# Performance work log

Hardware: AMD Instinct MI355X
Metric: run time of the kernel (lower is better)

Reference implementation:

```python
import jax, jax.numpy as jnp
import numpy as np

CHEB_K = 3


def cheb_gcn(x, node_emb, w_pool, b_pool):
    # x: [B, N, C], node_emb: [N, D], w_pool: [D, K, C, O], b_pool: [D, O]
    n = node_emb.shape[0]
    A = jax.nn.softmax(jax.nn.relu(node_emb @ node_emb.T), axis=1)  # [N, N]
    supports = [jnp.eye(n, dtype=x.dtype), A]
    for _ in range(2, CHEB_K):
        supports.append(2.0 * A @ supports[-1] - supports[-2])
    S = jnp.stack(supports, axis=0)  # [K, N, N]
    weights = jnp.einsum('nd,dkio->nkio', node_emb, w_pool)  # [N, K, C, O]
    bias = node_emb @ b_pool  # [N, O]
    x_g = jnp.einsum('knm,bmc->bnkc', S, x)  # [B, N, K, C]
    return jnp.einsum('bnki,nkio->bno', x_g, weights) + bias


def setup_inputs() -> dict:
    key = jax.random.key(0)
    ks = jax.random.split(key, 7)
    B, N, DIN, DOUT, E = 64, 1024, 64, 64, 16
    C = DIN + DOUT
    return {
        'x': jax.random.normal(ks[0], (B, N, DIN), jnp.float32),
        'state': jax.random.normal(ks[1], (B, N, DOUT), jnp.float32),
        'node_embeddings': jax.random.normal(ks[2], (N, E), jnp.float32),
        'W_gate': jax.random.normal(ks[3], (E, CHEB_K, C, 2 * DOUT), jnp.float32) * 0.1,
        'b_gate': jax.random.normal(ks[4], (E, 2 * DOUT), jnp.float32) * 0.1,
        'W_update': jax.random.normal(ks[5], (E, CHEB_K, C, DOUT), jnp.float32) * 0.1,
        'b_update': jax.random.normal(ks[6], (E, DOUT), jnp.float32) * 0.1,
    }


def reference(x, state, node_embeddings, W_gate, b_gate, W_update, b_update):
    hidden = state.shape[-1]
    inp = jnp.concatenate([x, state], axis=-1)  # [B, N, DIN+DOUT]
    z_r = jax.nn.sigmoid(cheb_gcn(inp, node_embeddings, W_gate, b_gate))
    z, r = z_r[..., :hidden], z_r[..., hidden:]
    cand = jnp.concatenate([x, r * state], axis=-1)
    h_hat = jnp.tanh(cheb_gcn(cand, node_embeddings, W_update, b_update))
    return z * state + (1.0 - z) * h_hat
```

## Files before the change

### kernel.cpp

```cpp
#include <hip/hip_runtime.h>
#include <hip/hip_bf16.h>
#include <math.h>

#define B_ 64
#define N_ 1024
#define E_ 16

typedef unsigned short ushort_t;
typedef __attribute__((ext_vector_type(8))) short bf16x8;
typedef __attribute__((ext_vector_type(4))) float f32x4;

__device__ __forceinline__ float sigmoidf_(float x) {
  return 1.0f / (1.0f + __expf(-x));
}
__device__ __forceinline__ ushort_t f2bf(float f) {
  unsigned int u = __float_as_uint(f);
  u = (u + 0x7fffu + ((u >> 16) & 1u)) >> 16;
  return (ushort_t)u;
}
__device__ __forceinline__ float bf2f(ushort_t h) { return __uint_as_float((unsigned)h << 16); }
__device__ __forceinline__ void gload16(const void* g, void* l) {
  __builtin_amdgcn_global_load_lds(
      (const __attribute__((address_space(1))) unsigned int*)g,
      (__attribute__((address_space(3))) unsigned int*)l, 16, 0, 0);
}

__global__ __launch_bounds__(256) void compute_A_kernel(const float* __restrict__ emb,
                                                        ushort_t* __restrict__ Ah,
                                                        ushort_t* __restrict__ Al) {
  __shared__ float embn[E_];
  __shared__ float red[256];
  const int n = blockIdx.x;
  const int t = threadIdx.x;
  if (t < E_) embn[t] = emb[n * E_ + t];
  __syncthreads();
  float s[4];
#pragma unroll
  for (int j = 0; j < 4; ++j) {
    const int m = j * 256 + t;
    const float* em = emb + m * E_;
    float acc = 0.f;
#pragma unroll
    for (int d = 0; d < E_; ++d) acc = fmaf(embn[d], em[d], acc);
    s[j] = fmaxf(acc, 0.f);
  }
  float mx = fmaxf(fmaxf(s[0], s[1]), fmaxf(s[2], s[3]));
  red[t] = mx;
  __syncthreads();
  for (int off = 128; off > 0; off >>= 1) {
    if (t < off) red[t] = fmaxf(red[t], red[t + off]);
    __syncthreads();
  }
  mx = red[0];
  __syncthreads();
  float e[4], lsum = 0.f;
#pragma unroll
  for (int j = 0; j < 4; ++j) { e[j] = __expf(s[j] - mx); lsum += e[j]; }
  red[t] = lsum;
  __syncthreads();
  for (int off = 128; off > 0; off >>= 1) {
    if (t < off) red[t] += red[t + off];
    __syncthreads();
  }
  const float inv = 1.0f / red[0];
#pragma unroll
  for (int j = 0; j < 4; ++j) {
    const float v = e[j] * inv;
    ushort_t h = f2bf(v);
    Ah[n * N_ + j * 256 + t] = h;
    Al[n * N_ + j * 256 + t] = f2bf(v - bf2f(h));
  }
}

__global__ __launch_bounds__(256) void transpose_A_kernel(const ushort_t* __restrict__ src1,
                                                          ushort_t* __restrict__ dst1,
                                                          const ushort_t* __restrict__ src2,
                                                          ushort_t* __restrict__ dst2) {
  __shared__ ushort_t tile[128][130];
  const int t = threadIdx.x;
  const int r0 = blockIdx.y << 7, c0 = blockIdx.x << 7;
  const ushort_t* src = src1;
  ushort_t* dst = dst1;
#pragma unroll
  for (int p = 0; p < 2; ++p) {
    if (p) { src = src2; dst = dst2; __syncthreads(); }
#pragma unroll
    for (int it = 0; it < 8; ++it) {
      const int id = it * 256 + t;
      const int row = id >> 4, ch = (id & 15) << 3;
      *(uint4*)&tile[row][ch] = *(const uint4*)&src[(size_t)(r0 + row) * 1024 + c0 + ch];
    }
    __syncthreads();
#pragma unroll
    for (int it = 0; it < 8; ++it) {
      const int id = it * 256 + t;
      const int row = id >> 4, ch = (id & 15) << 3;
      ushort_t v[8];
#pragma unroll
      for (int u = 0; u < 8; ++u) v[u] = tile[ch + u][row];
      *(uint4*)&dst[(size_t)(c0 + row) * 1024 + r0 + ch] = *(const uint4*)v;
    }
    __syncthreads();
  }
}

__global__ __launch_bounds__(256) void build_T0t_kernel(const float* __restrict__ xA,
                                                        const float* __restrict__ xB,
                                                        ushort_t* __restrict__ Th,
                                                        ushort_t* __restrict__ Tl) {
  __shared__ float tile[128][129];
  const int t = threadIdx.x;
  const int b = blockIdx.y;
  const int n0 = blockIdx.x << 7;
  const int c4 = (t & 31) << 2, nl = t >> 5;
#pragma unroll
  for (int p = 0; p < 16; ++p) {
    const int n = nl + (p << 3);
    const float4 v = (c4 < 64)
        ? *(const float4*)&xA[((size_t)b << 16) + ((size_t)(n0 + n) << 6) + c4]
        : *(const float4*)&xB[((size_t)b << 16) + ((size_t)(n0 + n) << 6) + c4 - 64];
    tile[c4 + 0][n] = v.x; tile[c4 + 1][n] = v.y;
    tile[c4 + 2][n] = v.z; tile[c4 + 3][n] = v.w;
  }
  __syncthreads();
  const int c = t >> 1, nc = (t & 1) << 6;
  const size_t obase = ((size_t)(b << 7) + c) * 1024 + n0 + nc;
#pragma unroll
  for (int u = 0; u < 64; u += 4) {
    ushort4 h, l;
    float v0 = tile[c][nc + u + 0], v1 = tile[c][nc + u + 1];
    float v2 = tile[c][nc + u + 2], v3 = tile[c][nc + u + 3];
    h.x = f2bf(v0); l.x = f2bf(v0 - bf2f(h.x));
    h.y = f2bf(v1); l.y = f2bf(v1 - bf2f(h.y));
    h.z = f2bf(v2); l.z = f2bf(v2 - bf2f(h.z));
    h.w = f2bf(v3); l.w = f2bf(v3 - bf2f(h.w));
    *(ushort4*)&Th[obase + u] = h;
    *(ushort4*)&Tl[obase + u] = l;
  }
}

__global__ __launch_bounds__(256) void build_T0s_kernel(const float* __restrict__ rs,
                                                        ushort_t* __restrict__ Th,
                                                        ushort_t* __restrict__ Tl) {
  __shared__ float tile[64][129];
  const int t = threadIdx.x;
  const int b = blockIdx.y;
  const int n0 = blockIdx.x << 7;
  const int c4 = (t & 15) << 2, nl = t >> 4;
#pragma unroll
  for (int p = 0; p < 8; ++p) {
    const int n = nl + (p << 4);
    const float4 v = *(const float4*)&rs[((size_t)b << 16) + ((size_t)(n0 + n) << 6) + c4];
    tile[c4 + 0][n] = v.x; tile[c4 + 1][n] = v.y;
    tile[c4 + 2][n] = v.z; tile[c4 + 3][n] = v.w;
  }
  __syncthreads();
  const int c = t >> 2, nc = (t & 3) << 5;
  const size_t obase = ((size_t)(b << 6) + c) * 1024 + n0 + nc;
#pragma unroll
  for (int u = 0; u < 32; u += 4) {
    ushort4 h, l;
    float v0 = tile[c][nc + u + 0], v1 = tile[c][nc + u + 1];
    float v2 = tile[c][nc + u + 2], v3 = tile[c][nc + u + 3];
    h.x = f2bf(v0); l.x = f2bf(v0 - bf2f(h.x));
    h.y = f2bf(v1); l.y = f2bf(v1 - bf2f(h.y));
    h.z = f2bf(v2); l.z = f2bf(v2 - bf2f(h.z));
    h.w = f2bf(v3); l.w = f2bf(v3 - bf2f(h.w));
    *(ushort4*)&Th[obase + u] = h;
    *(ushort4*)&Tl[obase + u] = l;
  }
}

template <int MODE, int SPAN>
__global__ __launch_bounds__(256, 2) void mfma_gemm_kernel(
    const ushort_t* __restrict__ Ah, const ushort_t* __restrict__ Al,
    const ushort_t* __restrict__ Bh, const ushort_t* __restrict__ Bl,
    ushort_t* __restrict__ OutH, ushort_t* __restrict__ OutL) {
  __shared__ ushort_t smem[4 * 128 * 64];
  ushort_t* Ah_s = smem;
  ushort_t* Al_s = smem + 8192;
  ushort_t* Bh_s = smem + 16384;
  ushort_t* Bl_s = smem + 24576;
  const int t = threadIdx.x;
  const int wave = t >> 6, lane = t & 63;
  const int n0 = blockIdx.y << 7;
  const int bcol = blockIdx.x;
  const int j0 = bcol << 7;
  const int wr = wave >> 1, wc = wave & 1;
  const int fr = lane & 15, fk = lane >> 4;

  f32x4 acc[4][4];
#pragma unroll
  for (int i = 0; i < 4; ++i)
#pragma unroll
    for (int j = 0; j < 4; ++j) acc[i][j] = (f32x4){0.f, 0.f, 0.f, 0.f};

  const int rsub = lane >> 3;
  const int cp = lane & 7;
  const int selem = (((cp << 4) ^ (rsub << 4)) >> 1);

  for (int k0 = 0; k0 < 1024; k0 += 64) {
    __syncthreads();
#pragma unroll
    for (int i = 0; i < 4; ++i) {
      const int q = (wave << 2) + i;
      const int row = (q << 3) + rsub;
      const int lo = (q << 9) + lane * 8;
      const size_t ga = (size_t)(n0 + row) * 1024 + k0 + selem;
      const size_t gb = (size_t)(j0 + row) * 1024 + k0 + selem;
      gload16(Ah + ga, Ah_s + lo);
      gload16(Al + ga, Al_s + lo);
      gload16(Bh + gb, Bh_s + lo);
      gload16(Bl + gb, Bl_s + lo);
    }
    __syncthreads();
#pragma unroll
    for (int ks = 0; ks < 2; ++ks) {
      bf16x8 ah[4], al[4], bh[4], bl[4];
#pragma unroll
      for (int mi = 0; mi < 4; ++mi) {
        const int r = (wr << 6) + (mi << 4) + fr;
        const int kb = ((ks << 6) + (fk << 4)) ^ ((r & 7) << 4);
        ah[mi] = *(const bf16x8*)((const char*)Ah_s + r * 128 + kb);
        al[mi] = *(const bf16x8*)((const char*)Al_s + r * 128 + kb);
      }
#pragma unroll
      for (int nj = 0; nj < 4; ++nj) {
        const int r = (wc << 6) + (nj << 4) + fr;
        const int kb = ((ks << 6) + (fk << 4)) ^ ((r & 7) << 4);
        bh[nj] = *(const bf16x8*)((const char*)Bh_s + r * 128 + kb);
        bl[nj] = *(const bf16x8*)((const char*)Bl_s + r * 128 + kb);
      }
#pragma unroll
      for (int mi = 0; mi < 4; ++mi)
#pragma unroll
        for (int nj = 0; nj < 4; ++nj) {
          acc[mi][nj] = __builtin_amdgcn_mfma_f32_16x16x32_bf16(ah[mi], bh[nj], acc[mi][nj], 0, 0, 0);
          acc[mi][nj] = __builtin_amdgcn_mfma_f32_16x16x32_bf16(ah[mi], bl[nj], acc[mi][nj], 0, 0, 0);
          acc[mi][nj] = __builtin_amdgcn_mfma_f32_16x16x32_bf16(al[mi], bh[nj], acc[mi][nj], 0, 0, 0);
        }
    }
  }

  __syncthreads();
  ushort_t* hiT = smem;
  ushort_t* loT = smem + 16384;
#pragma unroll
  for (int mi = 0; mi < 4; ++mi) {
    const int nl = (wr << 6) + (mi << 4) + (fk << 2);
#pragma unroll
    for (int nj = 0; nj < 4; ++nj) {
      const int jl = (wc << 6) + (nj << 4) + fr;
      const f32x4 vv = acc[mi][nj];
#pragma unroll
      for (int r = 0; r < 4; ++r) {
        const float v = (MODE == 1) ? 2.0f * vv[r] : vv[r];
        const ushort_t h = f2bf(v);
        hiT[(nl + r) * 128 + jl] = h;
        loT[(nl + r) * 128 + jl] = f2bf(v - bf2f(h));
      }
    }
  }
  __syncthreads();
  const int soff = (n0 >= 1024) ? 128 : 0;
  const int n0e = n0 & 1023;
#pragma unroll
  for (int rr = 0; rr < 8; ++rr) {
    const int id = rr * 256 + t;
    const int nl = id >> 4, ch = id & 15;
    size_t dstE;
    if (MODE == 1) {
      dstE = (size_t)(n0 + nl) * 1024 + j0 + ch * 8;
    } else if (SPAN == 128) {
      dstE = ((size_t)(n0e + nl) * 64 + bcol) * 256 + soff + ch * 8;
    } else {
      const int bb = bcol * 2 + (ch >> 3);
      dstE = ((size_t)(n0e + nl) * 64 + bb) * 256 + soff + 64 + (ch & 7) * 8;
    }
    *(uint4*)&OutH[dstE] = *(const uint4*)((const char*)hiT + nl * 256 + ch * 16);
    *(uint4*)&OutL[dstE] = *(const uint4*)((const char*)loT + nl * 256 + ch * 16);
  }
}

template <int OW>
__global__ __launch_bounds__(256) void wpt_kernel(const float* __restrict__ Wp,
                                                  float* __restrict__ WpT) {
  const int idx = blockIdx.x * 256 + threadIdx.x;
  const int ki = idx % 384;
  const int k = ki >> 7, i = ki & 127;
  const int o = idx / 384;
  float v[16];
#pragma unroll
  for (int d = 0; d < 16; ++d) v[d] = Wp[((size_t)d * 384 + ki) * OW + o];
  if (k == 0) {
#pragma unroll
    for (int d = 0; d < 16; ++d) v[d] -= Wp[((size_t)d * 384 + 256 + i) * OW + o];
  }
  float* dst = WpT + (size_t)idx * 16;
#pragma unroll
  for (int q = 0; q < 4; ++q) *(float4*)&dst[q * 4] = *(const float4*)&v[q * 4];
}

__global__ __launch_bounds__(384) void wcombine5_kernel(const float* __restrict__ emb,
                                                        const float* __restrict__ WpT,
                                                        ushort_t* __restrict__ WtH,
                                                        ushort_t* __restrict__ WtL) {
  __shared__ float embs[256 * 16];
  __shared__ ushort_t sH[8 * 384];
  __shared__ ushort_t sL[8 * 384];
  const int t = threadIdx.x;
  const int o = blockIdx.y;
  const int n0 = blockIdx.x << 8;
  for (int i = t; i < 1024; i += 384)
    *(float4*)&embs[i * 4] = *(const float4*)&emb[(size_t)n0 * 16 + i * 4];
  float wreg[16];
  {
    const float* src = WpT + (size_t)o * 6144 + t * 16;
#pragma unroll
    for (int q = 0; q < 4; ++q) *(float4*)&wreg[q * 4] = *(const float4*)&src[q * 4];
  }
  __syncthreads();
  for (int g = 0; g < 32; ++g) {
#pragma unroll
    for (int nl = 0; nl < 8; ++nl) {
      const float* e = &embs[(g * 8 + nl) * 16];
      float a = 0.f;
#pragma unroll
      for (int d = 0; d < 16; ++d) a = fmaf(e[d], wreg[d], a);
      const ushort_t h = f2bf(a);
      sH[nl * 384 + t] = h;
      sL[nl * 384 + t] = f2bf(a - bf2f(h));
    }
    __syncthreads();
    const size_t ob = ((size_t)o * 1024 + n0 + g * 8) * 384 + t * 8;
    *(uint4*)&WtH[ob] = *(const uint4*)&sH[t * 8];
    *(uint4*)&WtL[ob] = *(const uint4*)&sL[t * 8];
    __syncthreads();
  }
}

template <int MODE>
__global__ __launch_bounds__(256, 2) void pernode_mfma_kernel(
    const float* __restrict__ xA, const float* __restrict__ xB,
    const ushort_t* __restrict__ XpH, const ushort_t* __restrict__ XpL,
    const ushort_t* __restrict__ WtH, const ushort_t* __restrict__ WtL,
    const float* __restrict__ emb, const float* __restrict__ bsrc, int bstride,
    const float* __restrict__ state, const float* __restrict__ zb,
    float* __restrict__ dst) {
  __shared__ ushort_t xh_s[64 * 128];
  __shared__ ushort_t xl_s[64 * 128];
  __shared__ ushort_t wh_s[64 * 128];
  __shared__ ushort_t wl_s[64 * 128];
  __shared__ float embn[E_];
  __shared__ float bias[64];
  const int n = blockIdx.x;
  const int t = threadIdx.x;
  if (t < E_) embn[t] = emb[n * E_ + t];
  __syncthreads();
  if (t < 64) {
    float a = 0.f;
#pragma unroll
    for (int d = 0; d < E_; ++d) a = fmaf(embn[d], bsrc[d * bstride + t], a);
    bias[t] = a;
  }
  const int wave = t >> 6, lane = t & 63;
  const int fr = lane & 15, fq = lane >> 4;
  f32x4 acc[4];
#pragma unroll
  for (int i = 0; i < 4; ++i) acc[i] = (f32x4){0.f, 0.f, 0.f, 0.f};

#pragma unroll
  for (int s = 0; s < 3; ++s) {
    __syncthreads();
    if (s == 0) {
      const int b = t >> 2, q = t & 3;
      const float* srcp = (q < 2)
          ? xA + ((size_t)b << 16) + ((size_t)n << 6) + (q << 5)
          : xB + ((size_t)b << 16) + ((size_t)n << 6) + ((q - 2) << 5);
      float v[32];
#pragma unroll
      for (int j = 0; j < 8; ++j) *(float4*)&v[j * 4] = *(const float4*)&srcp[j * 4];
      const int swz = (b & 7) << 4;
#pragma unroll
      for (int jc = 0; jc < 4; ++jc) {
        unsigned int hh[4], ll[4];
#pragma unroll
        for (int e = 0; e < 4; ++e) {
          const float a0 = v[jc * 8 + 2 * e], a1 = v[jc * 8 + 2 * e + 1];
          const ushort_t h0 = f2bf(a0), h1 = f2bf(a1);
          const ushort_t l0 = f2bf(a0 - bf2f(h0)), l1 = f2bf(a1 - bf2f(h1));
          hh[e] = (unsigned)h0 | ((unsigned)h1 << 16);
          ll[e] = (unsigned)l0 | ((unsigned)l1 << 16);
        }
        const int dstb = b * 256 + (((q << 6) + (jc << 4)) ^ swz);
        *(uint4*)((char*)xh_s + dstb) = make_uint4(hh[0], hh[1], hh[2], hh[3]);
        *(uint4*)((char*)xl_s + dstb) = make_uint4(ll[0], ll[1], ll[2], ll[3]);
      }
    } else {
#pragma unroll
      for (int r = 0; r < 4; ++r) {
        const int id = r * 256 + t;
        const int row = id >> 4, ch = id & 15;
        const int selem = (((ch << 4) ^ ((row & 7) << 4)) >> 1);
        const size_t so = ((size_t)n * 64 + row) * 256 + (s - 1) * 128 + selem;
        gload16(XpH + so, xh_s + id * 8);
        gload16(XpL + so, xl_s + id * 8);
      }
    }
#pragma unroll
    for (int r = 0; r < 4; ++r) {
      const int id = r * 256 + t;
      const int row = id >> 4, ch = id & 15;
      const int selem = (((ch << 4) ^ ((row & 7) << 4)) >> 1);
      const size_t so = ((size_t)row * 1024 + n) * 384 + s * 128 + selem;
      gload16(WtH + so, wh_s + id * 8);
      gload16(WtL + so, wl_s + id * 8);
    }
    __syncthreads();
#pragma unroll
    for (int ks = 0; ks < 4; ++ks) {
      bf16x8 ah[4], al[4];
#pragma unroll
      for (int mi = 0; mi < 4; ++mi) {
        const int r = (mi << 4) + fr;
        const int kb = ((ks << 6) + (fq << 4)) ^ ((r & 7) << 4);
        ah[mi] = *(const bf16x8*)((const char*)xh_s + r * 256 + kb);
        al[mi] = *(const bf16x8*)((const char*)xl_s + r * 256 + kb);
      }
      const int rw = (wave << 4) + fr;
      const int kbw = ((ks << 6) + (fq << 4)) ^ ((rw & 7) << 4);
      const bf16x8 wh = *(const bf16x8*)((const char*)wh_s + rw * 256 + kbw);
      const bf16x8 wl = *(const bf16x8*)((const char*)wl_s + rw * 256 + kbw);
#pragma unroll
      for (int mi = 0; mi < 4; ++mi) {
        acc[mi] = __builtin_amdgcn_mfma_f32_16x16x32_bf16(ah[mi], wh, acc[mi], 0, 0, 0);
        acc[mi] = __builtin_amdgcn_mfma_f32_16x16x32_bf16(al[mi], wh, acc[mi], 0, 0, 0);
        acc[mi] = __builtin_amdgcn_mfma_f32_16x16x32_bf16(ah[mi], wl, acc[mi], 0, 0, 0);
      }
    }
  }

  const int o = (wave << 4) + fr;
  const float bia = bias[o];
#pragma unroll
  for (int mi = 0; mi < 4; ++mi) {
    const int b0 = (mi << 4) + (fq << 2);
    const f32x4 vv = acc[mi];
#pragma unroll
    for (int r = 0; r < 4; ++r) {
      const int b = b0 + r;
      const size_t base = ((size_t)b << 16) + ((size_t)n << 6);
      const float a = vv[r] + bia;
      if (MODE == 0) {
        dst[base + o] = sigmoidf_(a);
      } else if (MODE == 1) {
        dst[base + o] = sigmoidf_(a) * state[base + o];
      } else {
        const float z = zb[base + o], st = state[base + o];
        dst[base + o] = z * st + (1.f - z) * tanhf(a);
      }
    }
  }
}

extern "C" void kernel_launch(void* const* d_in, const int* in_sizes, int n_in,
                              void* d_out, int out_size, void* d_ws, size_t ws_size,
                              hipStream_t stream) {
  const float* x     = (const float*)d_in[0];
  const float* state = (const float*)d_in[1];
  const float* emb   = (const float*)d_in[2];
  const float* Wg    = (const float*)d_in[3];
  const float* bg    = (const float*)d_in[4];
  const float* Wu    = (const float*)d_in[5];
  const float* bu    = (const float*)d_in[6];
  float* out = (float*)d_out;

  char* w = (char*)d_ws;
  ushort_t* AhS  = (ushort_t*)(w);
  ushort_t* AlS  = (ushort_t*)(w + ((size_t)4 << 20));
  ushort_t* Ath  = (ushort_t*)(w + ((size_t)8 << 20));
  ushort_t* Atl  = (ushort_t*)(w + ((size_t)10 << 20));
  ushort_t* T0th = (ushort_t*)(w + ((size_t)12 << 20));
  ushort_t* T0tl = (ushort_t*)(w + ((size_t)28 << 20));
  ushort_t* XpH  = (ushort_t*)(w + ((size_t)44 << 20));
  ushort_t* XpL  = (ushort_t*)(w + ((size_t)76 << 20));
  ushort_t* WtH  = (ushort_t*)(w + ((size_t)108 << 20));
  ushort_t* WtL  = (ushort_t*)(w + ((size_t)156 << 20));
  float*    rs   = (float*)(w + ((size_t)204 << 20));
  float*    WpTg = (float*)(w + ((size_t)220 << 20));
  float*    WpTu = (float*)(w + ((size_t)223 << 20));
  ushort_t* Mh = AhS + (size_t)1024 * 1024;
  ushort_t* Ml = AlS + (size_t)1024 * 1024;
  float* zb = out;

  const dim3 ggd(64, 16);
  const dim3 gud(32, 16);
  const dim3 gm(8, 8);
  const dim3 gt(8, 64);
  const dim3 gc(4, 64);

  compute_A_kernel<<<N_, 256, 0, stream>>>(emb, AhS, AlS);
  transpose_A_kernel<<<gm, 256, 0, stream>>>(AhS, Ath, AlS, Atl);
  mfma_gemm_kernel<1, 128><<<gm, 256, 0, stream>>>(AhS, AlS, Ath, Atl, Mh, Ml);
  wpt_kernel<128><<<192, 256, 0, stream>>>(Wg, WpTg);
  wpt_kernel<64><<<96, 256, 0, stream>>>(Wu, WpTu);

  build_T0t_kernel<<<gt, 256, 0, stream>>>(x, state, T0th, T0tl);
  mfma_gemm_kernel<0, 128><<<ggd, 256, 0, stream>>>(AhS, AlS, T0th, T0tl, XpH, XpL);
  wcombine5_kernel<<<gc, 384, 0, stream>>>(emb, WpTg, WtH, WtL);
  pernode_mfma_kernel<0><<<N_, 256, 0, stream>>>(x, state, XpH, XpL, WtH, WtL, emb, bg, 128,
                                                 state, nullptr, zb);
  wcombine5_kernel<<<gc, 384, 0, stream>>>(emb, WpTg + (size_t)64 * 6144, WtH, WtL);
  pernode_mfma_kernel<1><<<N_, 256, 0, stream>>>(x, state, XpH, XpL, WtH, WtL, emb, bg + 64, 128,
                                                 state, nullptr, rs);

  wcombine5_kernel<<<gc, 384, 0, stream>>>(emb, WpTu, WtH, WtL);
  build_T0s_kernel<<<gt, 256, 0, stream>>>(rs, T0th, T0tl);
  mfma_gemm_kernel<0, 64><<<gud, 256, 0, stream>>>(AhS, AlS, T0th, T0tl, XpH, XpL);
  pernode_mfma_kernel<2><<<N_, 256, 0, stream>>>(x, rs, XpH, XpL, WtH, WtL, emb, bu, 64,
                                                 state, zb, out);
}
```

Measured before the change: 480.9 us.

## Double-buffer LDS tiles in split-bf16 MFMA GEMM with K-step of 32

Reworks the main GEMM loop to use two LDS buffers with a K-step of 32 instead of one buffer with a K-step of 64. The next tile's global-to-LDS loads are issued before the MFMAs on the current tile, leaving one barrier per iteration. This should hide global load latency behind compute. The cost is twice as many iterations, each with a barrier and less compute per step, plus a new swizzle layout. The LDS footprint is unchanged.

Result: no change. 481.9 us (+0.2%).

```diff
diff --git a/kernel.cpp b/kernel.cpp
--- a/kernel.cpp
+++ b/kernel.cpp
@@ -176,18 +176,14 @@
     const ushort_t* __restrict__ Ah, const ushort_t* __restrict__ Al,
     const ushort_t* __restrict__ Bh, const ushort_t* __restrict__ Bl,
     ushort_t* __restrict__ OutH, ushort_t* __restrict__ OutL) {
-  __shared__ ushort_t smem[4 * 128 * 64];
-  ushort_t* Ah_s = smem;
-  ushort_t* Al_s = smem + 8192;
-  ushort_t* Bh_s = smem + 16384;
-  ushort_t* Bl_s = smem + 24576;
+  __shared__ ushort_t smem[2 * 4 * 4096];
   const int t = threadIdx.x;
   const int wave = t >> 6, lane = t & 63;
   const int n0 = blockIdx.y << 7;
   const int bcol = blockIdx.x;
   const int j0 = bcol << 7;
   const int wr = wave >> 1, wc = wave & 1;
-  const int fr = lane & 15, fk = lane >> 4;
+  const int fr = lane & 15, fq = lane >> 4;
 
   f32x4 acc[4][4];
 #pragma unroll
@@ -195,59 +191,65 @@
 #pragma unroll
     for (int j = 0; j < 4; ++j) acc[i][j] = (f32x4){0.f, 0.f, 0.f, 0.f};
 
-  const int rsub = lane >> 3;
-  const int cp = lane & 7;
-  const int selem = (((cp << 4) ^ (rsub << 4)) >> 1);
-
-  for (int k0 = 0; k0 < 1024; k0 += 64) {
-    __syncthreads();
-#pragma unroll
-    for (int i = 0; i < 4; ++i) {
-      const int q = (wave << 2) + i;
-      const int row = (q << 3) + rsub;
-      const int lo = (q << 9) + lane * 8;
-      const size_t ga = (size_t)(n0 + row) * 1024 + k0 + selem;
-      const size_t gb = (size_t)(j0 + row) * 1024 + k0 + selem;
-      gload16(Ah + ga, Ah_s + lo);
-      gload16(Al + ga, Al_s + lo);
-      gload16(Bh + gb, Bh_s + lo);
-      gload16(Bl + gb, Bl_s + lo);
-    }
-    __syncthreads();
-#pragma unroll
-    for (int ks = 0; ks < 2; ++ks) {
-      bf16x8 ah[4], al[4], bh[4], bl[4];
-#pragma unroll
-      for (int mi = 0; mi < 4; ++mi) {
-        const int r = (wr << 6) + (mi << 4) + fr;
-        const int kb = ((ks << 6) + (fk << 4)) ^ ((r & 7) << 4);
-        ah[mi] = *(const bf16x8*)((const char*)Ah_s + r * 128 + kb);
-        al[mi] = *(const bf16x8*)((const char*)Al_s + r * 128 + kb);
-      }
+  const int lr3 = lane >> 3;
+  const int cs = (lane & 7) ^ lr3;
+  const int rofs = (cs >> 2);
+  const int kkofs = (cs & 3) << 3;
+  auto STAGE = [&](int bsel, int kb) {
+#pragma unroll
+    for (int i = 0; i < 2; ++i) {
+      const int q = (wave << 1) + i;
+      const int v = (q << 3) + lr3;
+      const int r = (v << 1) + rofs;
+      const int lo = bsel * 16384 + q * 512 + lane * 8;
+      const size_t ga = (size_t)(n0 + r) * 1024 + kb + kkofs;
+      const size_t gb = (size_t)(j0 + r) * 1024 + kb + kkofs;
+      gload16(Ah + ga, smem + lo);
+      gload16(Al + ga, smem + 4096 + lo);
+      gload16(Bh + gb, smem + 8192 + lo);
+      gload16(Bl + gb, smem + 12288 + lo);
+    }
+  };
+  auto FRAG = [&](const ushort_t* arrbase, int r) -> bf16x8 {
+    const int v = r >> 1;
+    const int b = ((((r & 1) << 2) | fq) ^ (v & 7)) << 4;
+    return *(const bf16x8*)((const char*)arrbase + v * 128 + b);
+  };
+
+  STAGE(0, 0);
+  __syncthreads();
+  for (int k = 0; k < 32; ++k) {
+    if (k < 31) STAGE((k + 1) & 1, (k + 1) << 5);
+    const ushort_t* cb = smem + (k & 1) * 16384;
+    bf16x8 ah[4], al[4], bh[4], bl[4];
+#pragma unroll
+    for (int mi = 0; mi < 4; ++mi) {
+      const int r = (wr << 6) + (mi << 4) + fr;
+      ah[mi] = FRAG(cb, r);
+      al[mi] = FRAG(cb + 4096, r);
+    }
+#pragma unroll
+    for (int nj = 0; nj < 4; ++nj) {
+      const int r = (wc << 6) + (nj << 4) + fr;
+      bh[nj] = FRAG(cb + 8192, r);
+      bl[nj] = FRAG(cb + 12288, r);
+    }
+#pragma unroll
+    for (int mi = 0; mi < 4; ++mi)
 #pragma unroll
       for (int nj = 0; nj < 4; ++nj) {
-        const int r = (wc << 6) + (nj << 4) + fr;
-        const int kb = ((ks << 6) + (fk << 4)) ^ ((r & 7) << 4);
-        bh[nj] = *(const bf16x8*)((const char*)Bh_s + r * 128 + kb);
-        bl[nj] = *(const bf16x8*)((const char*)Bl_s + r * 128 + kb);
-      }
-#pragma unroll
-      for (int mi = 0; mi < 4; ++mi)
-#pragma unroll
-        for (int nj = 0; nj < 4; ++nj) {
-          acc[mi][nj] = __builtin_amdgcn_mfma_f32_16x16x32_bf16(ah[mi], bh[nj], acc[mi][nj], 0, 0, 0);
-          acc[mi][nj] = __builtin_amdgcn_mfma_f32_16x16x32_bf16(ah[mi], bl[nj], acc[mi][nj], 0, 0, 0);
-          acc[mi][nj] = __builtin_amdgcn_mfma_f32_16x16x32_bf16(al[mi], bh[nj], acc[mi][nj], 0, 0, 0);
-        }
-    }
-  }
-
-  __syncthreads();
+        acc[mi][nj] = __builtin_amdgcn_mfma_f32_16x16x32_bf16(ah[mi], bh[nj], acc[mi][nj], 0, 0, 0);
+        acc[mi][nj] = __builtin_amdgcn_mfma_f32_16x16x32_bf16(ah[mi], bl[nj], acc[mi][nj], 0, 0, 0);
+        acc[mi][nj] = __builtin_amdgcn_mfma_f32_16x16x32_bf16(al[mi], bh[nj], acc[mi][nj], 0, 0, 0);
+      }
+    __syncthreads();
+  }
+
   ushort_t* hiT = smem;
   ushort_t* loT = smem + 16384;
 #pragma unroll
   for (int mi = 0; mi < 4; ++mi) {
-    const int nl = (wr << 6) + (mi << 4) + (fk << 2);
+    const int nl = (wr << 6) + (mi << 4) + (fq << 2);
 #pragma unroll
     for (int nj = 0; nj < 4; ++nj) {
       const int jl = (wc << 6) + (nj << 4) + fr;
```

## Fuse per-node weight generation into pernode MFMA kernel and merge z/r passes

Applied to the files above, without the earlier changes.

Drops the separate wcombine5 kernel, which wrote per-node bf16 hi/lo weight tensors to global memory. Each pernode block now computes its node's weights on the fly from the embedding and the pre-transposed weight pool, and stores them straight into shared memory. The z and r gate halves are handled in one launch, so the x/Xp staging is loaded once for both output halves. This cuts large global write and read traffic and several launches. The cost is extra FMA work and reads of the transposed pool in every block, plus higher register pressure from the doubled accumulators.

Measured after the change: 844.0 us. 1.75x slower.

```diff
diff --git a/kernel.cpp b/kernel.cpp
--- a/kernel.cpp
+++ b/kernel.cpp
@@ -301,73 +301,38 @@
   for (int q = 0; q < 4; ++q) *(float4*)&dst[q * 4] = *(const float4*)&v[q * 4];
 }
 
-__global__ __launch_bounds__(384) void wcombine5_kernel(const float* __restrict__ emb,
-                                                        const float* __restrict__ WpT,
-                                                        ushort_t* __restrict__ WtH,
-                                                        ushort_t* __restrict__ WtL) {
-  __shared__ float embs[256 * 16];
-  __shared__ ushort_t sH[8 * 384];
-  __shared__ ushort_t sL[8 * 384];
-  const int t = threadIdx.x;
-  const int o = blockIdx.y;
-  const int n0 = blockIdx.x << 8;
-  for (int i = t; i < 1024; i += 384)
-    *(float4*)&embs[i * 4] = *(const float4*)&emb[(size_t)n0 * 16 + i * 4];
-  float wreg[16];
-  {
-    const float* src = WpT + (size_t)o * 6144 + t * 16;
-#pragma unroll
-    for (int q = 0; q < 4; ++q) *(float4*)&wreg[q * 4] = *(const float4*)&src[q * 4];
-  }
-  __syncthreads();
-  for (int g = 0; g < 32; ++g) {
-#pragma unroll
-    for (int nl = 0; nl < 8; ++nl) {
-      const float* e = &embs[(g * 8 + nl) * 16];
-      float a = 0.f;
-#pragma unroll
-      for (int d = 0; d < 16; ++d) a = fmaf(e[d], wreg[d], a);
-      const ushort_t h = f2bf(a);
-      sH[nl * 384 + t] = h;
-      sL[nl * 384 + t] = f2bf(a - bf2f(h));
-    }
-    __syncthreads();
-    const size_t ob = ((size_t)o * 1024 + n0 + g * 8) * 384 + t * 8;
-    *(uint4*)&WtH[ob] = *(const uint4*)&sH[t * 8];
-    *(uint4*)&WtL[ob] = *(const uint4*)&sL[t * 8];
-    __syncthreads();
-  }
-}
-
 template <int MODE>
-__global__ __launch_bounds__(256, 2) void pernode_mfma_kernel(
+__global__ __launch_bounds__(256, 2) void pernode_fused_kernel(
     const float* __restrict__ xA, const float* __restrict__ xB,
     const ushort_t* __restrict__ XpH, const ushort_t* __restrict__ XpL,
-    const ushort_t* __restrict__ WtH, const ushort_t* __restrict__ WtL,
-    const float* __restrict__ emb, const float* __restrict__ bsrc, int bstride,
+    const float* __restrict__ WpT,
+    const float* __restrict__ emb, const float* __restrict__ bsrc,
     const float* __restrict__ state, const float* __restrict__ zb,
-    float* __restrict__ dst) {
+    float* __restrict__ dst0, float* __restrict__ dst1) {
+  constexpr int NOH = (MODE == 0) ? 2 : 1;
   __shared__ ushort_t xh_s[64 * 128];
   __shared__ ushort_t xl_s[64 * 128];
   __shared__ ushort_t wh_s[64 * 128];
   __shared__ ushort_t wl_s[64 * 128];
-  __shared__ float embn[E_];
-  __shared__ float bias[64];
+  __shared__ float bias[NOH * 64];
   const int n = blockIdx.x;
   const int t = threadIdx.x;
-  if (t < E_) embn[t] = emb[n * E_ + t];
-  __syncthreads();
-  if (t < 64) {
+  float e[16];
+#pragma unroll
+  for (int d = 0; d < 16; ++d) e[d] = emb[n * 16 + d];
+  if (t < NOH * 64) {
     float a = 0.f;
 #pragma unroll
-    for (int d = 0; d < E_; ++d) a = fmaf(embn[d], bsrc[d * bstride + t], a);
+    for (int d = 0; d < E_; ++d) a = fmaf(e[d], bsrc[d * (NOH * 64) + t], a);
     bias[t] = a;
   }
   const int wave = t >> 6, lane = t & 63;
   const int fr = lane & 15, fq = lane >> 4;
-  f32x4 acc[4];
-#pragma unroll
-  for (int i = 0; i < 4; ++i) acc[i] = (f32x4){0.f, 0.f, 0.f, 0.f};
+  f32x4 acc[NOH][4];
+#pragma unroll
+  for (int oh = 0; oh < NOH; ++oh)
+#pragma unroll
+    for (int i = 0; i < 4; ++i) acc[oh][i] = (f32x4){0.f, 0.f, 0.f, 0.f};
 
 #pragma unroll
   for (int s = 0; s < 3; ++s) {
@@ -385,12 +350,12 @@
       for (int jc = 0; jc < 4; ++jc) {
         unsigned int hh[4], ll[4];
 #pragma unroll
-        for (int e = 0; e < 4; ++e) {
-          const float a0 = v[jc * 8 + 2 * e], a1 = v[jc * 8 + 2 * e + 1];
+        for (int ee = 0; ee < 4; ++ee) {
+          const float a0 = v[jc * 8 + 2 * ee], a1 = v[jc * 8 + 2 * ee + 1];
           const ushort_t h0 = f2bf(a0), h1 = f2bf(a1);
           const ushort_t l0 = f2bf(a0 - bf2f(h0)), l1 = f2bf(a1 - bf2f(h1));
-          hh[e] = (unsigned)h0 | ((unsigned)h1 << 16);
-          ll[e] = (unsigned)l0 | ((unsigned)l1 << 16);
+          hh[ee] = (unsigned)h0 | ((unsigned)h1 << 16);
+          ll[ee] = (unsigned)l0 | ((unsigned)l1 << 16);
         }
         const int dstb = b * 256 + (((q << 6) + (jc << 4)) ^ swz);
         *(uint4*)((char*)xh_s + dstb) = make_uint4(hh[0], hh[1], hh[2], hh[3]);
@@ -408,56 +373,84 @@
       }
     }
 #pragma unroll
-    for (int r = 0; r < 4; ++r) {
-      const int id = r * 256 + t;
-      const int row = id >> 4, ch = id & 15;
-      const int selem = (((ch << 4) ^ ((row & 7) << 4)) >> 1);
-      const size_t so = ((size_t)row * 1024 + n) * 384 + s * 128 + selem;
-      gload16(WtH + so, wh_s + id * 8);
-      gload16(WtL + so, wl_s + id * 8);
-    }
-    __syncthreads();
-#pragma unroll
-    for (int ks = 0; ks < 4; ++ks) {
-      bf16x8 ah[4], al[4];
-#pragma unroll
-      for (int mi = 0; mi < 4; ++mi) {
-        const int r = (mi << 4) + fr;
-        const int kb = ((ks << 6) + (fq << 4)) ^ ((r & 7) << 4);
-        ah[mi] = *(const bf16x8*)((const char*)xh_s + r * 256 + kb);
-        al[mi] = *(const bf16x8*)((const char*)xl_s + r * 256 + kb);
-      }
-      const int rw = (wave << 4) + fr;
-      const int kbw = ((ks << 6) + (fq << 4)) ^ ((rw & 7) << 4);
-      const bf16x8 wh = *(const bf16x8*)((const char*)wh_s + rw * 256 + kbw);
-      const bf16x8 wl = *(const bf16x8*)((const char*)wl_s + rw * 256 + kbw);
-#pragma unroll
-      for (int mi = 0; mi < 4; ++mi) {
-        acc[mi] = __builtin_amdgcn_mfma_f32_16x16x32_bf16(ah[mi], wh, acc[mi], 0, 0, 0);
-        acc[mi] = __builtin_amdgcn_mfma_f32_16x16x32_bf16(al[mi], wh, acc[mi], 0, 0, 0);
-        acc[mi] = __builtin_amdgcn_mfma_f32_16x16x32_bf16(ah[mi], wl, acc[mi], 0, 0, 0);
+    for (int oh = 0; oh < NOH; ++oh) {
+      __syncthreads();
+      {
+        const float* wp = WpT + (((size_t)oh * 64) * 384 + (size_t)s * 128) * 16;
+#pragma unroll
+        for (int c4 = 0; c4 < 4; ++c4) {
+          const int chunk = c4 * 256 + t;
+          const int o = chunk >> 4;
+          const int ch = chunk & 15;
+          const float* src = wp + ((size_t)o * 384 + ch * 8) * 16;
+          unsigned int hv[4], lv[4];
+#pragma unroll
+          for (int p = 0; p < 4; ++p) {
+            float a2[2];
+#pragma unroll
+            for (int ss = 0; ss < 2; ++ss) {
+              const float* wrow = src + (p * 2 + ss) * 16;
+              float a = 0.f;
+#pragma unroll
+              for (int d = 0; d < 16; d += 4) {
+                const float4 wv = *(const float4*)&wrow[d];
+                a = fmaf(e[d], wv.x, a); a = fmaf(e[d + 1], wv.y, a);
+                a = fmaf(e[d + 2], wv.z, a); a = fmaf(e[d + 3], wv.w, a);
+              }
+              a2[ss] = a;
+            }
+            const ushort_t h0 = f2bf(a2[0]), h1 = f2bf(a2[1]);
+            const ushort_t l0 = f2bf(a2[0] - bf2f(h0)), l1 = f2bf(a2[1] - bf2f(h1));
+            hv[p] = (unsigned)h0 | ((unsigned)h1 << 16);
+            lv[p] = (unsigned)l0 | ((unsigned)l1 << 16);
+          }
+          const int dstb = o * 256 + ((ch * 16) ^ ((o & 7) << 4));
+          *(uint4*)((char*)wh_s + dstb) = make_uint4(hv[0], hv[1], hv[2], hv[3]);
+          *(uint4*)((char*)wl_s + dstb) = make_uint4(lv[0], lv[1], lv[2], lv[3]);
+        }
+      }
+      __syncthreads();
+#pragma unroll
+      for (int ks = 0; ks < 4; ++ks) {
+        bf16x8 ah[4], al[4];
+#pragma unroll
+        for (int mi = 0; mi < 4; ++mi) {
+          const int r = (mi << 4) + fr;
+          const int kb = ((ks << 6) + (fq << 4)) ^ ((r & 7) << 4);
+          ah[mi] = *(const bf16x8*)((const char*)xh_s + r * 256 + kb);
+          al[mi] = *(const bf16x8*)((const char*)xl_s + r * 256 + kb);
+        }
+        const int rw = (wave << 4) + fr;
+        const int kbw = ((ks << 6) + (fq << 4)) ^ ((rw & 7) << 4);
+        const bf16x8 wh = *(const bf16x8*)((const char*)wh_s + rw * 256 + kbw);
+        const bf16x8 wl = *(const bf16x8*)((const char*)wl_s + rw * 256 + kbw);
+#pragma unroll
+        for (int mi = 0; mi < 4; ++mi) {
+          acc[oh][mi] = __builtin_amdgcn_mfma_f32_16x16x32_bf16(ah[mi], wh, acc[oh][mi], 0, 0, 0);
+          acc[oh][mi] = __builtin_amdgcn_mfma_f32_16x16x32_bf16(al[mi], wh, acc[oh][mi], 0, 0, 0);
+          acc[oh][mi] = __builtin_amdgcn_mfma_f32_16x16x32_bf16(ah[mi], wl, acc[oh][mi], 0, 0, 0);
+        }
       }
     }
   }
 
   const int o = (wave << 4) + fr;
-  const float bia = bias[o];
 #pragma unroll
   for (int mi = 0; mi < 4; ++mi) {
     const int b0 = (mi << 4) + (fq << 2);
-    const f32x4 vv = acc[mi];
 #pragma unroll
     for (int r = 0; r < 4; ++r) {
       const int b = b0 + r;
       const size_t base = ((size_t)b << 16) + ((size_t)n << 6);
-      const float a = vv[r] + bia;
       if (MODE == 0) {
-        dst[base + o] = sigmoidf_(a);
-      } else if (MODE == 1) {
-        dst[base + o] = sigmoidf_(a) * state[base + o];
+        const float az = acc[0][mi][r] + bias[o];
+        const float ar = acc[1][mi][r] + bias[64 + o];
+        dst0[base + o] = sigmoidf_(az);
+        dst1[base + o] = sigmoidf_(ar) * state[base + o];
       } else {
+        const float a = acc[0][mi][r] + bias[o];
         const float z = zb[base + o], st = state[base + o];
-        dst[base + o] = z * st + (1.f - z) * tanhf(a);
+        dst0[base + o] = z * st + (1.f - z) * tanhf(a);
       }
     }
   }
@@ -484,11 +477,9 @@
   ushort_t* T0tl = (ushort_t*)(w + ((size_t)28 << 20));
   ushort_t* XpH  = (ushort_t*)(w + ((size_t)44 << 20));
   ushort_t* XpL  = (ushort_t*)(w + ((size_t)76 << 20));
-  ushort_t* WtH  = (ushort_t*)(w + ((size_t)108 << 20));
-  ushort_t* WtL  = (ushort_t*)(w + ((size_t)156 << 20));
-  float*    rs   = (float*)(w + ((size_t)204 << 20));
-  float*    WpTg = (float*)(w + ((size_t)220 << 20));
-  float*    WpTu = (float*)(w + ((size_t)223 << 20));
+  float*    rs   = (float*)(w + ((size_t)108 << 20));
+  float*    WpTg = (float*)(w + ((size_t)124 << 20));
+  float*    WpTu = (float*)(w + ((size_t)127 << 20));
   ushort_t* Mh = AhS + (size_t)1024 * 1024;
   ushort_t* Ml = AlS + (size_t)1024 * 1024;
   float* zb = out;
@@ -497,7 +488,6 @@
   const dim3 gud(32, 16);
   const dim3 gm(8, 8);
   const dim3 gt(8, 64);
-  const dim3 gc(4, 64);
 
   compute_A_kernel<<<N_, 256, 0, stream>>>(emb, AhS, AlS);
   transpose_A_kernel<<<gm, 256, 0, stream>>>(AhS, Ath, AlS, Atl);
@@ -507,16 +497,11 @@
 
   build_T0t_kernel<<<gt, 256, 0, stream>>>(x, state, T0th, T0tl);
   mfma_gemm_kernel<0, 128><<<ggd, 256, 0, stream>>>(AhS, AlS, T0th, T0tl, XpH, XpL);
-  wcombine5_kernel<<<gc, 384, 0, stream>>>(emb, WpTg, WtH, WtL);
-  pernode_mfma_kernel<0><<<N_, 256, 0, stream>>>(x, state, XpH, XpL, WtH, WtL, emb, bg, 128,
-                                                 state, nullptr, zb);
-  wcombine5_kernel<<<gc, 384, 0, stream>>>(emb, WpTg + (size_t)64 * 6144, WtH, WtL);
-  pernode_mfma_kernel<1><<<N_, 256, 0, stream>>>(x, state, XpH, XpL, WtH, WtL, emb, bg + 64, 128,
-                                                 state, nullptr, rs);
-
-  wcombine5_kernel<<<gc, 384, 0, stream>>>(emb, WpTu, WtH, WtL);
+  pernode_fused_kernel<0><<<N_, 256, 0, stream>>>(x, state, XpH, XpL, WpTg, emb, bg,
+                                                  state, nullptr, zb, rs);
+
   build_T0s_kernel<<<gt, 256, 0, stream>>>(rs, T0th, T0tl);
   mfma_gemm_kernel<0, 64><<<gud, 256, 0, stream>>>(AhS, AlS, T0th, T0tl, XpH, XpL);
-  pernode_mfma_kernel<2><<<N_, 256, 0, stream>>>(x, rs, XpH, XpL, WtH, WtL, emb, bu, 64,
-                                                 state, zb, out);
-}
+  pernode_fused_kernel<1><<<N_, 256, 0, stream>>>(x, rs, XpH, XpL, WpTu, emb, bu,
+                                                  state, zb, out, nullptr);
+}
```
